# Optimization experiments

Hardware: AMD Instinct MI355X
Metric: run time of the kernel (lower is better)

The kernel has to match this reference:

```python
import jax, jax.numpy as jnp
import numpy as np

B, C, T, I, R = 32, 4, 512, 64, 1024
LEAK = 0.5          # reak_rate
DENSITY = 0.1       # reservoir_density
SPECTRAL_RADIUS = 0.95
W_SCALE = 1.0       # reservoir_weights_scale
IN_SCALE = 0.1      # input_weights_scale


def setup_inputs() -> dict:
    rng = np.random.default_rng(0)
    # reservoir weights: uniform, sparsified by density mask, rescaled so the
    # largest singular value equals the target spectral radius (as in __init__)
    W = rng.uniform(-W_SCALE, W_SCALE, (R, R)).astype(np.float32)
    mask = (rng.uniform(0.0, 1.0, (R, R)) < DENSITY).astype(np.float32)
    W = W * mask
    s_max = np.linalg.svd(W, compute_uv=False).max()
    W = W * (SPECTRAL_RADIUS / s_max)
    # input weights: [R, I*C]
    Wi = rng.uniform(-IN_SCALE, IN_SCALE, (R, I * C)).astype(np.float32)

    key = jax.random.key(0)
    x = jax.random.normal(key, (B, C, T, I), dtype=jnp.float32)
    return {
        "x": x,
        "input_weights": jnp.asarray(Wi),
        "reservoir_weights": jnp.asarray(W),
    }


def reference(x, input_weights, reservoir_weights):
    # x: [B, C, T, I]
    B_, C_, T_, I_ = x.shape
    R_ = reservoir_weights.shape[0]
    # precompute the input projection for all steps: u_t = flatten(x[:,:,t,:]) @ Wi.T
    xt = jnp.transpose(x, (2, 0, 1, 3)).reshape(T_, B_, C_ * I_)  # [T, B, C*I]
    U = xt @ input_weights.T                                       # [T, B, R]

    h0 = jnp.zeros((B_, C_, R_), dtype=x.dtype)  # per-channel reservoir state

    def step(h, u):
        # leaky-integrated reservoir update; input broadcasts over channels
        h_new = LEAK * jnp.tanh(u[:, None, :] + h @ reservoir_weights) + (1.0 - LEAK) * h
        return h_new, h_new

    _, hs = jax.lax.scan(step, h0, U)            # hs: [T, B, C, R]
    return jnp.transpose(hs, (1, 2, 0, 3))       # [B, C, T, R]
```

## Files before the change

kernel.cpp:

```cpp
#include <hip/hip_runtime.h>
#include <hip/hip_bf16.h>
#include <cstdint>
#include <cstddef>


typedef unsigned short u16;
typedef unsigned int   u32;
typedef unsigned long long u64;
typedef __bf16 bf16x8 __attribute__((ext_vector_type(8)));
typedef u64    u64x2  __attribute__((ext_vector_type(2)));
typedef float  f32x4  __attribute__((ext_vector_type(4)));
typedef float  f32x2  __attribute__((ext_vector_type(2)));

#define T_STEPS 512
#define NWG     256
#define TPB     256

#define OFF_WHI 0
#define OFF_U   (2*1024*1024)
#define OFF_HB  (OFF_U + (size_t)512*32*1024*4)
#define HB_BYTES ((size_t)128*2048)
#define OFF_BAR (OFF_HB + 2*HB_BYTES)

__device__ __forceinline__ u16 f2bf(float f) {
  u32 u = __builtin_bit_cast(u32, f);
  u += 0x7fffu + ((u >> 16) & 1u);
  return (u16)(u >> 16);
}
__device__ __forceinline__ float bf2f(u16 h) {
  u32 u = ((u32)h) << 16;
  return __builtin_bit_cast(float, u);
}
__device__ __forceinline__ void pinv(bf16x8& v) { asm volatile("" : "+v"(v)); }

__device__ __forceinline__ u32 AADD(u32* p, u32 v) {
  return __hip_atomic_fetch_add(p, v, __ATOMIC_RELAXED, __HIP_MEMORY_SCOPE_AGENT);
}
__device__ __forceinline__ u32 ALD(const u32* p) {
  return __hip_atomic_load(p, __ATOMIC_RELAXED, __HIP_MEMORY_SCOPE_AGENT);
}
__device__ __forceinline__ u64 ALD64(const u64* p) {
  return __hip_atomic_load(p, __ATOMIC_RELAXED, __HIP_MEMORY_SCOPE_AGENT);
}
__device__ __forceinline__ void AST(u32* p, u32 v) {
  __hip_atomic_store(p, v, __ATOMIC_RELAXED, __HIP_MEMORY_SCOPE_AGENT);
}

__global__ void prep_w(const float* __restrict__ W, u16* __restrict__ whi) {
  int n = blockIdx.y;
  int k = blockIdx.x * 256 + threadIdx.x;
  whi[n * 1024 + k] = f2bf(W[k * 1024 + n]);
}

__global__ void __launch_bounds__(256) prep_u2(const float* __restrict__ x,
                                               const float* __restrict__ Wi,
                                               float* __restrict__ U) {
  __shared__ __align__(16) u16 Ah[128 * 128];
  __shared__ __align__(16) u16 Al[128 * 128];
  const int tid = threadIdx.x;
  const int m0 = blockIdx.x << 7;
  const int n0 = blockIdx.y << 7;
  const int wv = tid >> 6, lane = tid & 63;
  const int fc = lane & 15, kb = lane >> 4;

  f32x4 acc[8][2];
#pragma unroll
  for (int mt = 0; mt < 8; ++mt) {
    acc[mt][0] = (f32x4){0.f, 0.f, 0.f, 0.f};
    acc[mt][1] = (f32x4){0.f, 0.f, 0.f, 0.f};
  }

  for (int hf = 0; hf < 2; ++hf) {
    __syncthreads();
#pragma unroll
    for (int s = 0; s < 16; ++s) {
      int f = (s << 8) + tid;
      int row = f >> 5, v = f & 31;
      int cl = v >> 4, i4 = (v & 15) << 2;
      int b = row & 31, t = (m0 + row) >> 5;
      float4 xv = *(const float4*)(x +
          ((size_t)((b << 2) | ((hf << 1) | cl)) * 512 + t) * 64 + i4);
      int byte = (row << 8) + (((cl << 7) + (i4 << 1)) ^ ((row & 7) << 4));
      u16* ph = (u16*)((char*)Ah + byte);
      u16* pl = (u16*)((char*)Al + byte);
      float vv[4] = {xv.x, xv.y, xv.z, xv.w};
#pragma unroll
      for (int e = 0; e < 4; ++e) {
        u16 hh = f2bf(vv[e]);
        ph[e] = hh;
        pl[e] = f2bf(vv[e] - bf2f(hh));
      }
    }
    bf16x8 Bh[2][4], Bl[2][4];
#pragma unroll
    for (int nt = 0; nt < 2; ++nt) {
      const float* wrow = Wi + (size_t)(n0 + (wv << 5) + (nt << 4) + fc) * 256;
#pragma unroll
      for (int kt = 0; kt < 4; ++kt) {
        int k = (hf << 7) + (kt << 5) + (kb << 3);
        float tmp[8];
        *(float4*)&tmp[0] = *(const float4*)(wrow + k);
        *(float4*)&tmp[4] = *(const float4*)(wrow + k + 4);
#pragma unroll
        for (int e = 0; e < 8; ++e) {
          u16 hh = f2bf(tmp[e]);
          Bh[nt][kt][e] = __builtin_bit_cast(__bf16, hh);
          Bl[nt][kt][e] = __builtin_bit_cast(__bf16, f2bf(tmp[e] - bf2f(hh)));
        }
      }
    }
    __syncthreads();
#pragma unroll
    for (int kt = 0; kt < 4; ++kt) {
      int kbyte = (kt << 6) + (kb << 4);
#pragma unroll
      for (int mt = 0; mt < 8; ++mt) {
        int row = (mt << 4) + fc;
        int byte = (row << 8) + (kbyte ^ ((row & 7) << 4));
        bf16x8 ah = *(const bf16x8*)((char*)Ah + byte);
        bf16x8 al = *(const bf16x8*)((char*)Al + byte);
#pragma unroll
        for (int nt = 0; nt < 2; ++nt) {
          acc[mt][nt] = __builtin_amdgcn_mfma_f32_16x16x32_bf16(ah, Bh[nt][kt], acc[mt][nt], 0, 0, 0);
          acc[mt][nt] = __builtin_amdgcn_mfma_f32_16x16x32_bf16(al, Bh[nt][kt], acc[mt][nt], 0, 0, 0);
          acc[mt][nt] = __builtin_amdgcn_mfma_f32_16x16x32_bf16(ah, Bl[nt][kt], acc[mt][nt], 0, 0, 0);
        }
      }
    }
  }
#pragma unroll
  for (int mt = 0; mt < 8; ++mt) {
    int mbase = m0 + (mt << 4) + (kb << 2);
    int n = n0 + (wv << 5) + fc;
#pragma unroll
    for (int nt = 0; nt < 2; ++nt)
#pragma unroll
      for (int r = 0; r < 4; ++r)
        U[(size_t)(mbase + r) * 1024 + n + (nt << 4)] = acc[mt][nt][r];
  }
}

__global__ void __launch_bounds__(TPB, 1) esn_scan(
    const u16* __restrict__ Whi, const float* __restrict__ U,
    u16* __restrict__ Hb, float* __restrict__ out, u32* __restrict__ bar) {
  __shared__ __align__(16) float red[8 * 64 * 4];
  __shared__ int sh_q, sh_j, sh_loc;

  const int tid = threadIdx.x;
  const int wv = tid >> 6, lane = tid & 63;
  const int mcol = lane & 15, kb = lane >> 4;

  if (tid == 0) {
    int xcd;
    asm volatile("s_getreg_b32 %0, hwreg(HW_REG_XCC_ID)" : "=s"(xcd));
    xcd &= 7;
    AADD(bar + xcd * 64, 1u);
    AADD(bar + 512, 1u);
    while (ALD(bar + 512) < (u32)NWG) __builtin_amdgcn_s_sleep(2);
    bool uni = true;
    for (int k = 0; k < 8; ++k) uni &= (ALD(bar + k * 64) == 32u);
    if (uni) {
      sh_q = xcd;
      sh_j = (int)AADD(bar + (9 + xcd) * 64, 1u);
      sh_loc = 1;
    } else {
      sh_q = blockIdx.x & 7;
      sh_j = blockIdx.x >> 3;
      sh_loc = 0;
    }
  }
  __syncthreads();
  const int q = sh_q, j = sh_j;
  const bool xlocal = (sh_loc != 0);
  const int r0 = q << 4, c0 = j << 5;

  bf16x8 bh[2][8];
#pragma unroll
  for (int nt = 0; nt < 2; ++nt) {
    const char* wb = (const char*)Whi + (size_t)(c0 + nt * 16 + mcol) * 2048
                     + wv * 512 + kb * 16;
#pragma unroll
    for (int kt = 0; kt < 8; ++kt)
      bh[nt][kt] = *(const bf16x8*)(wb + kt * 64);
  }
#pragma unroll
  for (int nt = 0; nt < 2; ++nt)
#pragma unroll
    for (int kt = 0; kt < 8; ++kt) pinv(bh[nt][kt]);

  const int row_l = tid >> 4;
  const int col0  = (tid & 15) * 2;
  const int grow  = r0 + row_l;
  const int ont   = col0 >> 4, oci = col0 & 15;
  const int okb   = row_l >> 2, orr = row_l & 3;
  u32* flags = bar + 2048 + q * 64;

  float hreg[2] = {0.f, 0.f};
  f32x2 uf = *(const f32x2*)(U + (size_t)(grow >> 2) * 1024 + c0 + col0);

  for (int t = 0; t < T_STEPS; ++t) {
    const char* hsrc = (const char*)Hb + (size_t)(t & 1) * HB_BYTES
                       + (size_t)(r0 + mcol) * 2048 + wv * 512 + kb * 16;
    bf16x8 av[8];
    if (xlocal) {
#pragma unroll
      for (int kt = 0; kt < 8; ++kt)
        av[kt] = *(const bf16x8*)(hsrc + kt * 64);
    } else {
#pragma unroll
      for (int kt = 0; kt < 8; ++kt) {
        u64x2 p;
        p.x = ALD64((const u64*)(hsrc + kt * 64));
        p.y = ALD64((const u64*)(hsrc + kt * 64 + 8));
        av[kt] = __builtin_bit_cast(bf16x8, p);
      }
    }

    f32x4 acc0 = {0.f, 0.f, 0.f, 0.f};
    f32x4 acc1 = {0.f, 0.f, 0.f, 0.f};
#pragma unroll
    for (int kt = 0; kt < 8; ++kt) {
      acc0 = __builtin_amdgcn_mfma_f32_16x16x32_bf16(av[kt], bh[0][kt], acc0, 0, 0, 0);
      acc1 = __builtin_amdgcn_mfma_f32_16x16x32_bf16(av[kt], bh[1][kt], acc1, 0, 0, 0);
    }

    *(f32x4*)&red[((wv * 2 + 0) * 64 + lane) * 4] = acc0;
    *(f32x4*)&red[((wv * 2 + 1) * 64 + lane) * 4] = acc1;
    __syncthreads();

    float z0 = 0.f, z1 = 0.f;
#pragma unroll
    for (int w = 0; w < 4; ++w) {
      z0 += red[((w * 2 + ont) * 64 + okb * 16 + oci + 0) * 4 + orr];
      z1 += red[((w * 2 + ont) * 64 + okb * 16 + oci + 1) * 4 + orr];
    }
    float hn0 = 0.5f * tanhf(z0 + uf.x) + 0.5f * hreg[0];
    float hn1 = 0.5f * tanhf(z1 + uf.y) + 0.5f * hreg[1];
    hreg[0] = hn0; hreg[1] = hn1;

    {
      u32 pk = (u32)f2bf(hn0) | ((u32)f2bf(hn1) << 16);
      u32* hdst = (u32*)((char*)Hb + (size_t)((t + 1) & 1) * HB_BYTES
                         + (size_t)grow * 2048 + (c0 + col0) * 2);
      if (xlocal) {
        *hdst = pk;
      } else {
        (void)__hip_atomic_exchange(hdst, pk, __ATOMIC_RELAXED,
                                    __HIP_MEMORY_SCOPE_AGENT);
      }
    }
    asm volatile("s_waitcnt vmcnt(0)" ::: "memory");
    __syncthreads();

    if (t < T_STEPS - 1) {
      if (tid == 0) {
        if (xlocal) *(volatile u32*)(flags + j) = (u32)(t + 1);
        else        AST(flags + j, (u32)(t + 1));
      }
    }

    {
      f32x2 o2; o2.x = hn0; o2.y = hn1;
      __builtin_nontemporal_store(o2,
          (f32x2*)(out + ((size_t)grow * 512 + t) * 1024 + c0 + col0));
    }
    if (t < T_STEPS - 1) {
      uf = *(const f32x2*)(U + ((size_t)(t + 1) * 32 + (grow >> 2)) * 1024 + c0 + col0);
      if (wv == 0) {
        u32 tgt = (u32)(t + 1);
        if (xlocal) {
          const u32* fp = flags + (lane & 31);
          while (true) {
            u32 v = ALD(fp);
            if (__all((int)(v >= tgt))) break;
          }
          asm volatile("buffer_inv\n\ts_waitcnt vmcnt(0)" ::: "memory");
        } else {
          while (true) {
            u32 v = ALD(flags + (lane & 31));
            if (__all((int)(v >= tgt))) break;
            __builtin_amdgcn_s_sleep(1);
          }
        }
      }
      __syncthreads();
    }
  }
}

extern "C" void kernel_launch(void* const* d_in, const int* in_sizes, int n_in,
                              void* d_out, int out_size, void* d_ws, size_t ws_size,
                              hipStream_t stream) {
  (void)in_sizes; (void)n_in; (void)out_size; (void)ws_size;
  const float* x  = (const float*)d_in[0];
  const float* Wi = (const float*)d_in[1];
  const float* W  = (const float*)d_in[2];
  float* out = (float*)d_out;

  char* ws  = (char*)d_ws;
  u16*  whi = (u16*)(ws + OFF_WHI);
  float* U  = (float*)(ws + OFF_U);
  u16*  hb  = (u16*)(ws + OFF_HB);
  u32*  bar = (u32*)(ws + OFF_BAR);

  (void)hipMemsetAsync(ws + OFF_HB, 0, 2 * HB_BYTES + 16384, stream);

  hipLaunchKernelGGL(prep_w, dim3(4, 1024), dim3(256), 0, stream, W, whi);
  hipLaunchKernelGGL(prep_u2, dim3(128, 8), dim3(256), 0, stream, x, Wi, U);
  hipLaunchKernelGGL(esn_scan, dim3(NWG), dim3(TPB), 0, stream,
                     whi, U, hb, out, bar);
}
```

Measured before the change: 1.419 ms.

## Halve scan workgroups, give each wave full-K output tiles, drop LDS reduction and block barriers

The persistent scan kernel drops from 256 to 128 workgroups. Each wave now owns a 16x16 output tile over the full K=1024 and keeps 32 weight fragments in registers, so the LDS cross-wave reduction and the __syncthreads calls disappear. Every wave publishes its own flag and polls all 64 per-wave flags, which makes the step-to-step sync per wave instead of per block. The next U value is prefetched before the tanh. In exchange there are more register fragments and a longer serial MFMA chain per wave, and each wave polls more flags.

```diff
diff --git a/kernel.cpp b/kernel.cpp
--- a/kernel.cpp
+++ b/kernel.cpp
@@ -10,10 +10,9 @@
 typedef __bf16 bf16x8 __attribute__((ext_vector_type(8)));
 typedef u64    u64x2  __attribute__((ext_vector_type(2)));
 typedef float  f32x4  __attribute__((ext_vector_type(4)));
-typedef float  f32x2  __attribute__((ext_vector_type(2)));
 
 #define T_STEPS 512
-#define NWG     256
+#define NWG     128
 #define TPB     256
 
 #define OFF_WHI 0
@@ -143,12 +142,11 @@
 __global__ void __launch_bounds__(TPB, 1) esn_scan(
     const u16* __restrict__ Whi, const float* __restrict__ U,
     u16* __restrict__ Hb, float* __restrict__ out, u32* __restrict__ bar) {
-  __shared__ __align__(16) float red[8 * 64 * 4];
   __shared__ int sh_q, sh_j, sh_loc;
 
   const int tid = threadIdx.x;
   const int wv = tid >> 6, lane = tid & 63;
-  const int mcol = lane & 15, kb = lane >> 4;
+  const int fc = lane & 15, kb = lane >> 4;
 
   if (tid == 0) {
     int xcd;
@@ -158,7 +156,7 @@
     AADD(bar + 512, 1u);
     while (ALD(bar + 512) < (u32)NWG) __builtin_amdgcn_s_sleep(2);
     bool uni = true;
-    for (int k = 0; k < 8; ++k) uni &= (ALD(bar + k * 64) == 32u);
+    for (int k = 0; k < 8; ++k) uni &= (ALD(bar + k * 64) == 16u);
     if (uni) {
       sh_q = xcd;
       sh_j = (int)AADD(bar + (9 + xcd) * 64, 1u);
@@ -172,119 +170,105 @@
   __syncthreads();
   const int q = sh_q, j = sh_j;
   const bool xlocal = (sh_loc != 0);
-  const int r0 = q << 4, c0 = j << 5;
-
-  bf16x8 bh[2][8];
-#pragma unroll
-  for (int nt = 0; nt < 2; ++nt) {
-    const char* wb = (const char*)Whi + (size_t)(c0 + nt * 16 + mcol) * 2048
-                     + wv * 512 + kb * 16;
-#pragma unroll
-    for (int kt = 0; kt < 8; ++kt)
-      bh[nt][kt] = *(const bf16x8*)(wb + kt * 64);
-  }
-#pragma unroll
-  for (int nt = 0; nt < 2; ++nt)
-#pragma unroll
-    for (int kt = 0; kt < 8; ++kt) pinv(bh[nt][kt]);
-
-  const int row_l = tid >> 4;
-  const int col0  = (tid & 15) * 2;
-  const int grow  = r0 + row_l;
-  const int ont   = col0 >> 4, oci = col0 & 15;
-  const int okb   = row_l >> 2, orr = row_l & 3;
+  const int r0 = q << 4;
+  const int n0w = (j << 6) + (wv << 4);
+
+  const char* wb = (const char*)Whi + (size_t)(n0w + fc) * 2048 + (kb << 4);
+  bf16x8 wf[32];
+#pragma unroll
+  for (int kt = 0; kt < 32; ++kt)
+    wf[kt] = *(const bf16x8*)(wb + (kt << 6));
+#pragma unroll
+  for (int kt = 0; kt < 32; ++kt) pinv(wf[kt]);
+
+  const int grow = r0 + fc;
+  const int ncol = n0w + (kb << 2);
   u32* flags = bar + 2048 + q * 64;
-
-  float hreg[2] = {0.f, 0.f};
-  f32x2 uf = *(const f32x2*)(U + (size_t)(grow >> 2) * 1024 + c0 + col0);
+  const int slot = (j << 2) + wv;
+
+  float hreg[4] = {0.f, 0.f, 0.f, 0.f};
+  f32x4 uf = *(const f32x4*)(U + (size_t)(grow >> 2) * 1024 + ncol);
 
   for (int t = 0; t < T_STEPS; ++t) {
     const char* hsrc = (const char*)Hb + (size_t)(t & 1) * HB_BYTES
-                       + (size_t)(r0 + mcol) * 2048 + wv * 512 + kb * 16;
-    bf16x8 av[8];
+                       + (size_t)grow * 2048 + (kb << 4);
+    bf16x8 hf[32];
     if (xlocal) {
 #pragma unroll
-      for (int kt = 0; kt < 8; ++kt)
-        av[kt] = *(const bf16x8*)(hsrc + kt * 64);
+      for (int kt = 0; kt < 32; ++kt)
+        hf[kt] = *(const bf16x8*)(hsrc + (kt << 6));
     } else {
 #pragma unroll
-      for (int kt = 0; kt < 8; ++kt) {
+      for (int kt = 0; kt < 32; ++kt) {
         u64x2 p;
-        p.x = ALD64((const u64*)(hsrc + kt * 64));
-        p.y = ALD64((const u64*)(hsrc + kt * 64 + 8));
-        av[kt] = __builtin_bit_cast(bf16x8, p);
-      }
-    }
-
-    f32x4 acc0 = {0.f, 0.f, 0.f, 0.f};
-    f32x4 acc1 = {0.f, 0.f, 0.f, 0.f};
-#pragma unroll
-    for (int kt = 0; kt < 8; ++kt) {
-      acc0 = __builtin_amdgcn_mfma_f32_16x16x32_bf16(av[kt], bh[0][kt], acc0, 0, 0, 0);
-      acc1 = __builtin_amdgcn_mfma_f32_16x16x32_bf16(av[kt], bh[1][kt], acc1, 0, 0, 0);
-    }
-
-    *(f32x4*)&red[((wv * 2 + 0) * 64 + lane) * 4] = acc0;
-    *(f32x4*)&red[((wv * 2 + 1) * 64 + lane) * 4] = acc1;
-    __syncthreads();
-
-    float z0 = 0.f, z1 = 0.f;
-#pragma unroll
-    for (int w = 0; w < 4; ++w) {
-      z0 += red[((w * 2 + ont) * 64 + okb * 16 + oci + 0) * 4 + orr];
-      z1 += red[((w * 2 + ont) * 64 + okb * 16 + oci + 1) * 4 + orr];
-    }
-    float hn0 = 0.5f * tanhf(z0 + uf.x) + 0.5f * hreg[0];
-    float hn1 = 0.5f * tanhf(z1 + uf.y) + 0.5f * hreg[1];
-    hreg[0] = hn0; hreg[1] = hn1;
-
-    {
-      u32 pk = (u32)f2bf(hn0) | ((u32)f2bf(hn1) << 16);
-      u32* hdst = (u32*)((char*)Hb + (size_t)((t + 1) & 1) * HB_BYTES
-                         + (size_t)grow * 2048 + (c0 + col0) * 2);
+        p.x = ALD64((const u64*)(hsrc + (kt << 6)));
+        p.y = ALD64((const u64*)(hsrc + (kt << 6) + 8));
+        hf[kt] = __builtin_bit_cast(bf16x8, p);
+      }
+    }
+
+    f32x4 a0 = {0.f, 0.f, 0.f, 0.f}, a1 = {0.f, 0.f, 0.f, 0.f};
+    f32x4 a2 = {0.f, 0.f, 0.f, 0.f}, a3 = {0.f, 0.f, 0.f, 0.f};
+#pragma unroll
+    for (int kt = 0; kt < 32; kt += 4) {
+      a0 = __builtin_amdgcn_mfma_f32_16x16x32_bf16(wf[kt + 0], hf[kt + 0], a0, 0, 0, 0);
+      a1 = __builtin_amdgcn_mfma_f32_16x16x32_bf16(wf[kt + 1], hf[kt + 1], a1, 0, 0, 0);
+      a2 = __builtin_amdgcn_mfma_f32_16x16x32_bf16(wf[kt + 2], hf[kt + 2], a2, 0, 0, 0);
+      a3 = __builtin_amdgcn_mfma_f32_16x16x32_bf16(wf[kt + 3], hf[kt + 3], a3, 0, 0, 0);
+    }
+    f32x4 z = (a0 + a1) + (a2 + a3);
+
+    f32x4 ufn = uf;
+    if (t < T_STEPS - 1)
+      ufn = *(const f32x4*)(U + ((size_t)(t + 1) * 32 + (grow >> 2)) * 1024 + ncol);
+
+    f32x4 o;
+    u64 pk = 0;
+#pragma unroll
+    for (int r = 0; r < 4; ++r) {
+      float hn = 0.5f * tanhf(z[r] + uf[r]) + 0.5f * hreg[r];
+      hreg[r] = hn;
+      o[r] = hn;
+      pk |= (u64)f2bf(hn) << (16 * r);
+    }
+
+    u64* hdst = (u64*)((char*)Hb + (size_t)((t + 1) & 1) * HB_BYTES
+                       + (size_t)grow * 2048 + (size_t)ncol * 2);
+    __builtin_amdgcn_sched_barrier(0);
+    if (xlocal) {
+      *hdst = pk;
+    } else {
+      (void)__hip_atomic_exchange(hdst, pk, __ATOMIC_RELAXED,
+                                  __HIP_MEMORY_SCOPE_AGENT);
+    }
+    __builtin_amdgcn_sched_barrier(0);
+    __builtin_nontemporal_store(o,
+        (f32x4*)(out + ((size_t)grow * 512 + t) * 1024 + ncol));
+    __builtin_amdgcn_sched_barrier(0);
+
+    if (t < T_STEPS - 1) {
+      asm volatile("s_waitcnt vmcnt(1)" ::: "memory");
+      if (lane == 0) {
+        if (xlocal) *(volatile u32*)(flags + slot) = (u32)(t + 1);
+        else        AST(flags + slot, (u32)(t + 1));
+      }
+      u32 tgt = (u32)(t + 1);
       if (xlocal) {
-        *hdst = pk;
+        const u32* fp = flags + lane;
+        while (true) {
+          u32 v = ALD(fp);
+          if (__all((int)(v >= tgt))) break;
+        }
+        asm volatile("buffer_inv\n\ts_waitcnt vmcnt(0)" ::: "memory");
       } else {
-        (void)__hip_atomic_exchange(hdst, pk, __ATOMIC_RELAXED,
-                                    __HIP_MEMORY_SCOPE_AGENT);
-      }
-    }
-    asm volatile("s_waitcnt vmcnt(0)" ::: "memory");
-    __syncthreads();
-
-    if (t < T_STEPS - 1) {
-      if (tid == 0) {
-        if (xlocal) *(volatile u32*)(flags + j) = (u32)(t + 1);
-        else        AST(flags + j, (u32)(t + 1));
-      }
-    }
-
-    {
-      f32x2 o2; o2.x = hn0; o2.y = hn1;
-      __builtin_nontemporal_store(o2,
-          (f32x2*)(out + ((size_t)grow * 512 + t) * 1024 + c0 + col0));
-    }
-    if (t < T_STEPS - 1) {
-      uf = *(const f32x2*)(U + ((size_t)(t + 1) * 32 + (grow >> 2)) * 1024 + c0 + col0);
-      if (wv == 0) {
-        u32 tgt = (u32)(t + 1);
-        if (xlocal) {
-          const u32* fp = flags + (lane & 31);
-          while (true) {
-            u32 v = ALD(fp);
-            if (__all((int)(v >= tgt))) break;
-          }
-          asm volatile("buffer_inv\n\ts_waitcnt vmcnt(0)" ::: "memory");
-        } else {
-          while (true) {
-            u32 v = ALD(flags + (lane & 31));
-            if (__all((int)(v >= tgt))) break;
-            __builtin_amdgcn_s_sleep(1);
-          }
-        }
-      }
-      __syncthreads();
-    }
+        while (true) {
+          u32 v = ALD(flags + lane);
+          if (__all((int)(v >= tgt))) break;
+          __builtin_amdgcn_s_sleep(1);
+        }
+      }
+    }
+    uf = ufn;
   }
 }
 
```

After: 3.336 ms. 135% more time.

## Halve scan workgroups, widen per-WG column tile, and relax per-step cache sync

Applied to the files above, without the earlier changes.

The recurrent scan now runs on 128 workgroups instead of 256. Each workgroup computes a 16x64 slice of the state using four MFMA column tiles, so only 16 peers per row group have to be polled each step. The hidden-state load always uses atomic 64-bit loads. The buffer_inv and the explicit vmcnt wait before the barrier are dropped, and the next step's input projection is prefetched before the matrix multiply. The intent is to cut cross-workgroup synchronisation cost per timestep, at the price of more serial work per workgroup and weaker memory-ordering guarantees between the state writes and the flag publish.

```diff
diff --git a/kernel.cpp b/kernel.cpp
--- a/kernel.cpp
+++ b/kernel.cpp
@@ -10,10 +10,9 @@
 typedef __bf16 bf16x8 __attribute__((ext_vector_type(8)));
 typedef u64    u64x2  __attribute__((ext_vector_type(2)));
 typedef float  f32x4  __attribute__((ext_vector_type(4)));
-typedef float  f32x2  __attribute__((ext_vector_type(2)));
 
 #define T_STEPS 512
-#define NWG     256
+#define NWG     128
 #define TPB     256
 
 #define OFF_WHI 0
@@ -143,12 +142,12 @@
 __global__ void __launch_bounds__(TPB, 1) esn_scan(
     const u16* __restrict__ Whi, const float* __restrict__ U,
     u16* __restrict__ Hb, float* __restrict__ out, u32* __restrict__ bar) {
-  __shared__ __align__(16) float red[8 * 64 * 4];
+  __shared__ __align__(16) float red[4 * 4 * 64 * 4];
   __shared__ int sh_q, sh_j, sh_loc;
 
   const int tid = threadIdx.x;
   const int wv = tid >> 6, lane = tid & 63;
-  const int mcol = lane & 15, kb = lane >> 4;
+  const int mrow = lane & 15, kb = lane >> 4;
 
   if (tid == 0) {
     int xcd;
@@ -158,7 +157,7 @@
     AADD(bar + 512, 1u);
     while (ALD(bar + 512) < (u32)NWG) __builtin_amdgcn_s_sleep(2);
     bool uni = true;
-    for (int k = 0; k < 8; ++k) uni &= (ALD(bar + k * 64) == 32u);
+    for (int k = 0; k < 8; ++k) uni &= (ALD(bar + k * 64) == 16u);
     if (uni) {
       sh_q = xcd;
       sh_j = (int)AADD(bar + (9 + xcd) * 64, 1u);
@@ -172,84 +171,91 @@
   __syncthreads();
   const int q = sh_q, j = sh_j;
   const bool xlocal = (sh_loc != 0);
-  const int r0 = q << 4, c0 = j << 5;
-
-  bf16x8 bh[2][8];
-#pragma unroll
-  for (int nt = 0; nt < 2; ++nt) {
-    const char* wb = (const char*)Whi + (size_t)(c0 + nt * 16 + mcol) * 2048
+  const int r0 = q << 4, c0 = j << 6;
+
+  bf16x8 bh[4][8];
+#pragma unroll
+  for (int nt = 0; nt < 4; ++nt) {
+    const char* wb = (const char*)Whi + (size_t)(c0 + nt * 16 + mrow) * 2048
                      + wv * 512 + kb * 16;
 #pragma unroll
     for (int kt = 0; kt < 8; ++kt)
       bh[nt][kt] = *(const bf16x8*)(wb + kt * 64);
   }
 #pragma unroll
-  for (int nt = 0; nt < 2; ++nt)
+  for (int nt = 0; nt < 4; ++nt)
 #pragma unroll
     for (int kt = 0; kt < 8; ++kt) pinv(bh[nt][kt]);
 
   const int row_l = tid >> 4;
-  const int col0  = (tid & 15) * 2;
+  const int col4  = (tid & 15) << 2;
   const int grow  = r0 + row_l;
-  const int ont   = col0 >> 4, oci = col0 & 15;
+  const int ont   = col4 >> 4, ofc = col4 & 15;
   const int okb   = row_l >> 2, orr = row_l & 3;
   u32* flags = bar + 2048 + q * 64;
 
-  float hreg[2] = {0.f, 0.f};
-  f32x2 uf = *(const f32x2*)(U + (size_t)(grow >> 2) * 1024 + c0 + col0);
+  float hreg[4] = {0.f, 0.f, 0.f, 0.f};
+  f32x4 uf = *(const f32x4*)(U + (size_t)(grow >> 2) * 1024 + c0 + col4);
 
   for (int t = 0; t < T_STEPS; ++t) {
     const char* hsrc = (const char*)Hb + (size_t)(t & 1) * HB_BYTES
-                       + (size_t)(r0 + mcol) * 2048 + wv * 512 + kb * 16;
+                       + (size_t)(r0 + mrow) * 2048 + wv * 512 + kb * 16;
     bf16x8 av[8];
-    if (xlocal) {
-#pragma unroll
-      for (int kt = 0; kt < 8; ++kt)
-        av[kt] = *(const bf16x8*)(hsrc + kt * 64);
-    } else {
-#pragma unroll
-      for (int kt = 0; kt < 8; ++kt) {
-        u64x2 p;
-        p.x = ALD64((const u64*)(hsrc + kt * 64));
-        p.y = ALD64((const u64*)(hsrc + kt * 64 + 8));
-        av[kt] = __builtin_bit_cast(bf16x8, p);
-      }
-    }
-
-    f32x4 acc0 = {0.f, 0.f, 0.f, 0.f};
-    f32x4 acc1 = {0.f, 0.f, 0.f, 0.f};
 #pragma unroll
     for (int kt = 0; kt < 8; ++kt) {
-      acc0 = __builtin_amdgcn_mfma_f32_16x16x32_bf16(av[kt], bh[0][kt], acc0, 0, 0, 0);
-      acc1 = __builtin_amdgcn_mfma_f32_16x16x32_bf16(av[kt], bh[1][kt], acc1, 0, 0, 0);
-    }
-
-    *(f32x4*)&red[((wv * 2 + 0) * 64 + lane) * 4] = acc0;
-    *(f32x4*)&red[((wv * 2 + 1) * 64 + lane) * 4] = acc1;
+      u64x2 p;
+      p.x = ALD64((const u64*)(hsrc + kt * 64));
+      p.y = ALD64((const u64*)(hsrc + kt * 64 + 8));
+      av[kt] = __builtin_bit_cast(bf16x8, p);
+    }
+    f32x4 ufn = uf;
+    if (t < T_STEPS - 1)
+      ufn = *(const f32x4*)(U + ((size_t)(t + 1) * 32 + (grow >> 2)) * 1024 + c0 + col4);
+
+    f32x4 acc[4];
+#pragma unroll
+    for (int nt = 0; nt < 4; ++nt) acc[nt] = (f32x4){0.f, 0.f, 0.f, 0.f};
+#pragma unroll
+    for (int kt = 0; kt < 8; ++kt) {
+#pragma unroll
+      for (int nt = 0; nt < 4; ++nt)
+        acc[nt] = __builtin_amdgcn_mfma_f32_16x16x32_bf16(av[kt], bh[nt][kt], acc[nt], 0, 0, 0);
+    }
+
+#pragma unroll
+    for (int nt = 0; nt < 4; ++nt)
+      *(f32x4*)&red[((wv * 4 + nt) * 64 + lane) * 4] = acc[nt];
     __syncthreads();
 
-    float z0 = 0.f, z1 = 0.f;
+    f32x4 z = {0.f, 0.f, 0.f, 0.f};
 #pragma unroll
     for (int w = 0; w < 4; ++w) {
-      z0 += red[((w * 2 + ont) * 64 + okb * 16 + oci + 0) * 4 + orr];
-      z1 += red[((w * 2 + ont) * 64 + okb * 16 + oci + 1) * 4 + orr];
-    }
-    float hn0 = 0.5f * tanhf(z0 + uf.x) + 0.5f * hreg[0];
-    float hn1 = 0.5f * tanhf(z1 + uf.y) + 0.5f * hreg[1];
-    hreg[0] = hn0; hreg[1] = hn1;
+#pragma unroll
+      for (int i = 0; i < 4; ++i)
+        z[i] += red[((w * 4 + ont) * 64 + okb * 16 + ofc + i) * 4 + orr];
+    }
+    f32x4 o;
+    u64 pk = 0;
+#pragma unroll
+    for (int r = 0; r < 4; ++r) {
+      float hn = 0.5f * tanhf(z[r] + uf[r]) + 0.5f * hreg[r];
+      hreg[r] = hn;
+      o[r] = hn;
+      pk |= (u64)f2bf(hn) << (16 * r);
+    }
 
     {
-      u32 pk = (u32)f2bf(hn0) | ((u32)f2bf(hn1) << 16);
-      u32* hdst = (u32*)((char*)Hb + (size_t)((t + 1) & 1) * HB_BYTES
-                         + (size_t)grow * 2048 + (c0 + col0) * 2);
+      u64* hdst = (u64*)((char*)Hb + (size_t)((t + 1) & 1) * HB_BYTES
+                         + (size_t)grow * 2048 + (size_t)(c0 + col4) * 2);
       if (xlocal) {
         *hdst = pk;
       } else {
         (void)__hip_atomic_exchange(hdst, pk, __ATOMIC_RELAXED,
                                     __HIP_MEMORY_SCOPE_AGENT);
       }
-    }
-    asm volatile("s_waitcnt vmcnt(0)" ::: "memory");
+      __builtin_nontemporal_store(o,
+          (f32x4*)(out + ((size_t)grow * 512 + t) * 1024 + c0 + col4));
+    }
     __syncthreads();
 
     if (t < T_STEPS - 1) {
@@ -257,27 +263,17 @@
         if (xlocal) *(volatile u32*)(flags + j) = (u32)(t + 1);
         else        AST(flags + j, (u32)(t + 1));
       }
-    }
-
-    {
-      f32x2 o2; o2.x = hn0; o2.y = hn1;
-      __builtin_nontemporal_store(o2,
-          (f32x2*)(out + ((size_t)grow * 512 + t) * 1024 + c0 + col0));
-    }
-    if (t < T_STEPS - 1) {
-      uf = *(const f32x2*)(U + ((size_t)(t + 1) * 32 + (grow >> 2)) * 1024 + c0 + col0);
       if (wv == 0) {
         u32 tgt = (u32)(t + 1);
         if (xlocal) {
-          const u32* fp = flags + (lane & 31);
+          const u32* fp = flags + (lane & 15);
           while (true) {
             u32 v = ALD(fp);
             if (__all((int)(v >= tgt))) break;
           }
-          asm volatile("buffer_inv\n\ts_waitcnt vmcnt(0)" ::: "memory");
         } else {
           while (true) {
-            u32 v = ALD(flags + (lane & 31));
+            u32 v = ALD(flags + (lane & 15));
             if (__all((int)(v >= tgt))) break;
             __builtin_amdgcn_s_sleep(1);
           }
@@ -285,6 +281,7 @@
       }
       __syncthreads();
     }
+    uf = ufn;
   }
 }
 
```

New measurement: 1.862 ms. 1.31x slower.
